# Performance work log

Measured on AMD Instinct MI355X. Metric: run time of the kernel, lower is better.

The kernel has to match this reference:

```python
import jax, jax.numpy as jnp
import numpy as np

N = 30000
F_IN = 500
HID = 16
OUT = 3
E = 960000


def setup_inputs() -> dict:
    key = jax.random.key(0)
    ks = jax.random.split(key, 10)
    x = jax.random.normal(ks[0], (N, F_IN), dtype=jnp.float32)
    edge_index = jax.random.randint(ks[1], (2, E), 0, N, dtype=jnp.int32)
    # CNN params (torch Conv1d: weight [out, in, k], bias [out])
    s1 = 1.0 / np.sqrt(1 * 3)
    s2 = 1.0 / np.sqrt(HID * 3)
    conv1_w = jax.random.uniform(ks[2], (HID, 1, 3), jnp.float32, -s1, s1)
    conv1_b = jax.random.uniform(ks[3], (HID,), jnp.float32, -s1, s1)
    conv2_w = jax.random.uniform(ks[4], (HID, HID, 3), jnp.float32, -s2, s2)
    conv2_b = jax.random.uniform(ks[5], (HID,), jnp.float32, -s2, s2)
    # GCNConv params (glorot weight [in, out], zero bias)
    g1 = np.sqrt(6.0 / (HID + HID))
    g2 = np.sqrt(6.0 / (HID + OUT))
    gcn1_w = jax.random.uniform(ks[6], (HID, HID), jnp.float32, -g1, g1)
    gcn1_b = jnp.zeros((HID,), jnp.float32)
    gcn2_w = jax.random.uniform(ks[7], (HID, OUT), jnp.float32, -g2, g2)
    gcn2_b = jnp.zeros((OUT,), jnp.float32)
    return {"x": x, "conv1_w": conv1_w, "conv1_b": conv1_b,
            "conv2_w": conv2_w, "conv2_b": conv2_b,
            "gcn1_w": gcn1_w, "gcn1_b": gcn1_b,
            "gcn2_w": gcn2_w, "gcn2_b": gcn2_b,
            "edge_index": edge_index}


def _conv1d(x, w, b):
    # x: [N, C_in, L], w: [C_out, C_in, 3], padding=1
    y = jax.lax.conv_general_dilated(
        x, w, window_strides=(1,), padding=[(1, 1)],
        dimension_numbers=("NCH", "OIH", "NCH"))
    return y + b[None, :, None]


def _gcn_conv(x, w, b, src, dst, n):
    # x: [n, d_in] -> [n, d_out]; Kipf normalization with self-loops
    h = x @ w
    loop = jnp.arange(n, dtype=src.dtype)
    s = jnp.concatenate([src, loop])
    d = jnp.concatenate([dst, loop])
    deg = jax.ops.segment_sum(jnp.ones_like(d, dtype=h.dtype), d, num_segments=n)
    dinv = jnp.where(deg > 0, jax.lax.rsqrt(deg), 0.0)
    norm = dinv[s] * dinv[d]                      # [E+n]
    msg = h[s] * norm[:, None]                    # gather + scale
    return jax.ops.segment_sum(msg, d, num_segments=n) + b


def reference(x, conv1_w, conv1_b, conv2_w, conv2_b,
              gcn1_w, gcn1_b, gcn2_w, gcn2_b, edge_index):
    # CNN feature extractor over feature axis
    h = x[:, None, :]                             # [N, 1, F_IN]
    h = jax.nn.relu(_conv1d(h, conv1_w, conv1_b))  # [N, HID, F_IN]
    h = jax.nn.relu(_conv1d(h, conv2_w, conv2_b))  # [N, HID, F_IN]
    h = jnp.max(h, axis=2)                        # global max pool -> [N, HID]
    # GCN
    src, dst = edge_index[0], edge_index[1]
    n = h.shape[0]
    h = jax.nn.relu(_gcn_conv(h, gcn1_w, gcn1_b, src, dst, n))
    h = _gcn_conv(h, gcn2_w, gcn2_b, src, dst, n)  # [N, OUT]
    return jax.nn.log_softmax(h, axis=1)
```

## Files before the change

### kernel.cpp

```cpp
#include <hip/hip_runtime.h>
#include <hip/hip_bf16.h>

#define N_NODES 30000
#define F_INLEN 500
#define HID 16
#define OUTC 3
#define NEDGE 960000
#define YPITCH 20
#define NBIN 938
#define HBLK 128
#define EPRH (NEDGE / HBLK)
#define ECAP 1536
#define NPB2 235

typedef float  f32x4 __attribute__((ext_vector_type(4)));
typedef float  f32x2 __attribute__((ext_vector_type(2)));
typedef short  s16x8 __attribute__((ext_vector_type(8)));

static __device__ __forceinline__ unsigned short f2bf(float f) {
    unsigned int u = __float_as_uint(f);
    unsigned int r = (u + 0x7fffu + ((u >> 16) & 1u)) >> 16;
    return (unsigned short)r;
}
static __device__ __forceinline__ unsigned int pack_bf16x2(float v0, float v1) {
#if __has_builtin(__builtin_amdgcn_cvt_pk_bf16_f32)
    typedef __bf16 bf16x2_t __attribute__((ext_vector_type(2)));
    union { bf16x2_t v; unsigned int u; } cv;
    cv.v = __builtin_amdgcn_cvt_pk_bf16_f32(v0, v1);
    return cv.u;
#else
    return __builtin_amdgcn_perm(__float_as_uint(v1), __float_as_uint(v0), 0x07060302);
#endif
}

__global__ void setup_kernel(const float* __restrict__ w2, short* __restrict__ bfragsG,
                             int* __restrict__ degi)
{
    const int tid = threadIdx.x;
    const int gid = blockIdx.x * 256 + tid;
    if (gid < N_NODES) degi[gid] = 0;
    if (blockIdx.x == 0 && tid < 64) {
        const int n16 = tid & 15, q = tid >> 4;
#pragma unroll
        for (int j = 0; j < 8; j++) {
            {
                const int c = q * 8 + j;
                const int t = c >> 4, i = c & 15;
                bfragsG[tid * 16 + j] = (short)f2bf(w2[n16 * 48 + i * 3 + t]);
            }
            {
                const int c = 32 + q * 8 + j;
                short v = 0;
                if (c < 48) { const int t = c >> 4, i = c & 15; v = (short)f2bf(w2[n16 * 48 + i * 3 + t]); }
                bfragsG[tid * 16 + 8 + j] = v;
            }
        }
    }
}

__global__ __launch_bounds__(256, 7) void conv_hist(
    const float* __restrict__ x,
    const float* __restrict__ w1, const float* __restrict__ b1,
    const float* __restrict__ b2, const short* __restrict__ bfragsG,
    const int* __restrict__ dst, int* __restrict__ degi,
    int* __restrict__ cntbase, float* __restrict__ h0)
{
    __shared__ __align__(16) float xp[502];
    __shared__ __align__(16) unsigned short yh[516 * YPITCH];
    __shared__ float red[64];

    const int tid = threadIdx.x;

    if (blockIdx.x < HBLK) {
        int* histH = (int*)yh;
        for (int i = tid; i < NBIN; i += 256) histH[i] = 0;
        __syncthreads();
        const int e0 = blockIdx.x * EPRH;
        for (int e = e0 + tid; e < e0 + EPRH; e += 256) {
            const int d = dst[e];
            atomicAdd(&histH[d >> 5], 1);
            atomicAdd(&degi[d], 1);
        }
        __syncthreads();
        for (int i = tid; i < NBIN; i += 256) cntbase[blockIdx.x * NBIN + i] = histH[i];
        return;
    }

    const int node = blockIdx.x - HBLK;
    const int lane = tid & 63;
    const int wave = tid >> 6;
    const int n16  = lane & 15;
    const int q    = lane >> 4;

    if (tid == 0) { xp[0] = 0.f; xp[501] = 0.f; }
    if (tid < 125) {
        const float4 v = ((const float4*)(x + (long long)node * F_INLEN))[tid];
        xp[4 * tid + 1] = v.x; xp[4 * tid + 2] = v.y;
        xp[4 * tid + 3] = v.z; xp[4 * tid + 4] = v.w;
    }
    {
        const int ri = tid >> 4;
        const int row = (ri == 0) ? 0 : (500 + ri);
        yh[row * YPITCH + (tid & 15)] = 0;
    }
    const s16x8* bfp = (const s16x8*)(bfragsG + lane * 16);
    const s16x8 bh0 = bfp[0], bh1 = bfp[1];

    f32x2 wt0[8], wt1[8], wt2[8], bb[8];
#pragma unroll
    for (int cp = 0; cp < 8; cp++) {
        const int c0 = 2 * cp, c1 = 2 * cp + 1;
        wt0[cp] = (f32x2){w1[c0 * 3 + 0], w1[c1 * 3 + 0]};
        wt1[cp] = (f32x2){w1[c0 * 3 + 1], w1[c1 * 3 + 1]};
        wt2[cp] = (f32x2){w1[c0 * 3 + 2], w1[c1 * 3 + 2]};
        bb[cp]  = (f32x2){b1[c0], b1[c1]};
    }
    __syncthreads();

    for (int p = tid; p < 500; p += 256) {
        const float x0 = xp[p], x1 = xp[p + 1], x2 = xp[p + 2];
        const f32x2 xv0 = {x0, x0}, xv1 = {x1, x1}, xv2 = {x2, x2};
        const f32x2 zero = {0.f, 0.f};
        unsigned int hp[8];
#pragma unroll
        for (int cp = 0; cp < 8; cp++) {
            f32x2 a = bb[cp];
            a = __builtin_elementwise_fma(wt0[cp], xv0, a);
            a = __builtin_elementwise_fma(wt1[cp], xv1, a);
            a = __builtin_elementwise_fma(wt2[cp], xv2, a);
            a = __builtin_elementwise_max(a, zero);
            hp[cp] = pack_bf16x2(a[0], a[1]);
        }
        uint2* d = (uint2*)&yh[(p + 1) * YPITCH];
        d[0] = make_uint2(hp[0], hp[1]);
        d[1] = make_uint2(hp[2], hp[3]);
        d[2] = make_uint2(hp[4], hp[5]);
        d[3] = make_uint2(hp[6], hp[7]);
    }
    __syncthreads();

    struct S8 { short4 lo, hi; };
    float mx0 = -3.0e38f, mx1 = -3.0e38f, mx2 = -3.0e38f, mx3 = -3.0e38f;
#pragma unroll
    for (int it = 0; it < 8; it++) {
        const int tile = wave * 8 + it;
        const int p0 = tile * 16 + n16;
        const int cA = (q & 1) * 8;
        const int rA = p0 + (q >> 1);
        const int rB = p0 + 2 + (q >> 1);
        S8 t0, t1;
        t0.lo = *(const short4*)&yh[rA * YPITCH + cA];
        t0.hi = *(const short4*)&yh[rA * YPITCH + cA + 4];
        t1.lo = *(const short4*)&yh[rB * YPITCH + cA];
        t1.hi = *(const short4*)&yh[rB * YPITCH + cA + 4];
        const s16x8 ah0 = *(const s16x8*)&t0;
        const s16x8 ah1 = *(const s16x8*)&t1;
        f32x4 acc = {0.f, 0.f, 0.f, 0.f};
        acc = __builtin_amdgcn_mfma_f32_16x16x32_bf16(ah0, bh0, acc, 0, 0, 0);
        acc = __builtin_amdgcn_mfma_f32_16x16x32_bf16(ah1, bh1, acc, 0, 0, 0);
        if (it < 7) {
            mx0 = fmaxf(mx0, acc[0]);
            mx1 = fmaxf(mx1, acc[1]);
            mx2 = fmaxf(mx2, acc[2]);
            mx3 = fmaxf(mx3, acc[3]);
        } else if (wave < 3) {
            mx0 = fmaxf(mx0, acc[0]);
            mx1 = fmaxf(mx1, acc[1]);
            mx2 = fmaxf(mx2, acc[2]);
            mx3 = fmaxf(mx3, acc[3]);
        } else if (q == 0) {
            mx0 = fmaxf(mx0, acc[0]);
            mx1 = fmaxf(mx1, acc[1]);
            mx2 = fmaxf(mx2, acc[2]);
            mx3 = fmaxf(mx3, acc[3]);
        }
    }
    float m = fmaxf(fmaxf(mx0, mx1), fmaxf(mx2, mx3));
    m = fmaxf(m, __shfl_xor(m, 16));
    m = fmaxf(m, __shfl_xor(m, 32));
    if (lane < 16) red[wave * 16 + lane] = m;
    __syncthreads();
    if (tid < 16) {
        const float mm = fmaxf(fmaxf(red[tid], red[16 + tid]), fmaxf(red[32 + tid], red[48 + tid]));
        h0[node * HID + tid] = fmaxf(mm + b2[tid], 0.f);
    }
}

__global__ __launch_bounds__(512) void reorder2(
    const int* __restrict__ src, const int* __restrict__ dst,
    const int* __restrict__ cntbase, int* __restrict__ packed,
    int* __restrict__ binstart, const int* __restrict__ degi,
    float* __restrict__ dinv, float* __restrict__ h0)
{
    __shared__ int2 sc2A[NBIN], sc2B[NBIN];
    __shared__ int gexc[NBIN];
    __shared__ int lexc[NBIN];
    __shared__ int cursor[NBIN];
    __shared__ int srt[EPRH];
    const int tid = threadIdx.x;
    const int blk = blockIdx.x;

    for (int bin = tid; bin < NBIN; bin += 512) {
        int tot = 0, psum = 0, lc = 0;
        for (int k = 0; k < HBLK; k++) {
            const int c = cntbase[k * NBIN + bin];
            tot += c;
            if (k < blk) psum += c;
            if (k == blk) lc = c;
        }
        cursor[bin] = tot;
        gexc[bin]   = psum;
        lexc[bin]   = lc;
        sc2A[bin]   = make_int2(tot, lc);
    }
    __syncthreads();
    {
        int2* pA = sc2A; int2* pB = sc2B;
        for (int off = 1; off < NBIN; off <<= 1) {
            for (int i = tid; i < NBIN; i += 512) {
                int2 v = pA[i];
                if (i >= off) { const int2 u = pA[i - off]; v.x += u.x; v.y += u.y; }
                pB[i] = v;
            }
            __syncthreads();
            int2* tp = pA; pA = pB; pB = tp;
        }
        for (int i = tid; i < NBIN; i += 512) {
            const int tot = cursor[i];
            const int lc  = lexc[i];
            const int et  = pA[i].x - tot;
            const int el  = pA[i].y - lc;
            gexc[i] += et;
            if (blk == 0) binstart[i] = et;
            lexc[i]   = el;
            cursor[i] = el;
        }
        if (blk == 0 && tid == 0) binstart[NBIN] = NEDGE;
    }
    __syncthreads();
    const int e0 = blk * EPRH;
    for (int e = e0 + tid; e < e0 + EPRH; e += 512) {
        const int d = dst[e];
        const int bin = d >> 5;
        const int pos = atomicAdd(&cursor[bin], 1);
        srt[pos] = src[e] | (d << 15);
    }
    __syncthreads();
    for (int i = tid; i < EPRH; i += 512) {
        const int bin = srt[i] >> 20;
        packed[gexc[bin] + (i - lexc[bin])] = srt[i];
    }
    const int n0 = blk * NPB2;
    for (int n = n0 + tid; n < n0 + NPB2 && n < N_NODES; n += 512) {
        const float dv = rsqrtf((float)(degi[n] + 1));
        dinv[n] = dv;
        f32x4* h4 = (f32x4*)(h0 + n * HID);
#pragma unroll
        for (int k = 0; k < 4; k++) h4[k] = h4[k] * dv;
    }
}

__global__ __launch_bounds__(256) void agg1_kernel(
    const int* __restrict__ binstart, const int* __restrict__ packed,
    const float* __restrict__ h0,
    const float* __restrict__ W1, const float* __restrict__ b1g,
    const float* __restrict__ W2, float4* __restrict__ t2p4)
{
    __shared__ float w1s[256];
    __shared__ float w2s[48];
    __shared__ float b1s[16];
    __shared__ float accS[32 * 17];
    __shared__ int eL[ECAP];
    __shared__ int srt[ECAP];
    __shared__ int h32[32], ls32[32], lofs32[32];
    const int tid = threadIdx.x;
    const int blk = blockIdx.x;
    w1s[tid] = W1[tid];
    if (tid < 48) w2s[tid] = W2[tid];
    if (tid < 16) b1s[tid] = b1g[tid];
    if (tid < 32) h32[tid] = 0;
    const int beg = binstart[blk];
    const int cnt = binstart[blk + 1] - beg;
    __syncthreads();
    for (int j = tid; j < cnt; j += 256) {
        const int p = packed[beg + j];
        eL[j] = p;
        atomicAdd(&h32[(p >> 15) & 31], 1);
    }
    __syncthreads();
    if (tid < 32) {
        const int v = h32[tid];
        int inc = v;
#pragma unroll
        for (int off = 1; off < 32; off <<= 1) {
            const int y = __shfl_up(inc, off);
            if (tid >= off) inc += y;
        }
        ls32[tid] = inc - v;
        lofs32[tid] = inc - v;
    }
    __syncthreads();
    for (int j = tid; j < cnt; j += 256) {
        const int p = eL[j];
        const int pos = atomicAdd(&lofs32[(p >> 15) & 31], 1);
        srt[pos] = p;
    }
    __syncthreads();
    const int n = tid >> 3;
    const int eslot = (tid >> 2) & 1;
    const int q = tid & 3;
    const int node = blk * 32 + n;
    const bool valid = node < N_NODES;
    f32x4 acc = {0.f, 0.f, 0.f, 0.f};
    if (valid) {
        const int s0 = ls32[n];
        const int s1 = s0 + h32[n];
        for (int i = s0 + eslot; i < s1; i += 2) {
            const int s = srt[i] & 32767;
            acc += *(const f32x4*)(h0 + s * HID + q * 4);
        }
    }
#pragma unroll
    for (int c = 0; c < 4; c++) acc[c] += __shfl_xor(acc[c], 4);
    if (valid && eslot == 0) {
        acc += *(const f32x4*)(h0 + node * HID + q * 4);
        accS[n * 17 + q * 4 + 0] = acc[0];
        accS[n * 17 + q * 4 + 1] = acc[1];
        accS[n * 17 + q * 4 + 2] = acc[2];
        accS[n * 17 + q * 4 + 3] = acc[3];
    }
    __syncthreads();
    if (tid < 128) {
        const int n2 = tid >> 2;
        const int node2 = blk * 32 + n2;
        if (node2 < N_NODES) {
            const float dv = rsqrtf((float)(h32[n2] + 1));
            const int q2 = tid & 3;
            float y0 = 0.f, y1 = 0.f, y2 = 0.f, y3 = 0.f;
#pragma unroll
            for (int i = 0; i < 16; i++) {
                const float a = accS[n2 * 17 + i];
                y0 = fmaf(a, w1s[i * 16 + q2 * 4 + 0], y0);
                y1 = fmaf(a, w1s[i * 16 + q2 * 4 + 1], y1);
                y2 = fmaf(a, w1s[i * 16 + q2 * 4 + 2], y2);
                y3 = fmaf(a, w1s[i * 16 + q2 * 4 + 3], y3);
            }
            float d0 = 0.f, d1 = 0.f, d2 = 0.f;
            const float yv[4] = {y0, y1, y2, y3};
#pragma unroll
            for (int j = 0; j < 4; j++) {
                const int o = q2 * 4 + j;
                const float h = fmaxf(b1s[o] + dv * yv[j], 0.f);
                d0 = fmaf(h, w2s[o * 3 + 0], d0);
                d1 = fmaf(h, w2s[o * 3 + 1], d1);
                d2 = fmaf(h, w2s[o * 3 + 2], d2);
            }
            d0 += __shfl_xor(d0, 1); d0 += __shfl_xor(d0, 2);
            d1 += __shfl_xor(d1, 1); d1 += __shfl_xor(d1, 2);
            d2 += __shfl_xor(d2, 1); d2 += __shfl_xor(d2, 2);
            if (q2 == 0) t2p4[node2] = make_float4(d0 * dv, d1 * dv, d2 * dv, dv);
        }
    }
}

__global__ __launch_bounds__(256) void agg2_kernel(
    const int* __restrict__ binstart, const int* __restrict__ packed,
    const float4* __restrict__ t2p4,
    const float* __restrict__ b2g, float* __restrict__ out)
{
    __shared__ float acc2[32 * 5];
    const int tid = threadIdx.x;
    const int blk = blockIdx.x;
    for (int i = tid; i < 32 * 5; i += 256) acc2[i] = 0.f;
    const int beg = binstart[blk];
    const int end = binstart[blk + 1];
    __syncthreads();
    for (int j = beg + tid; j < end; j += 256) {
        const int p = packed[j];
        const int s = p & 32767;
        const int dl = (p >> 15) & 31;
        const float4 v = t2p4[s];
        atomicAdd(&acc2[dl * 5 + 0], v.x);
        atomicAdd(&acc2[dl * 5 + 1], v.y);
        atomicAdd(&acc2[dl * 5 + 2], v.z);
    }
    __syncthreads();
    if (tid < 32) {
        const int node = blk * 32 + tid;
        if (node < N_NODES) {
            const float4 self = t2p4[node];
            const float dv = self.w;
            const float z0 = b2g[0] + dv * (acc2[tid * 5 + 0] + self.x);
            const float z1 = b2g[1] + dv * (acc2[tid * 5 + 1] + self.y);
            const float z2 = b2g[2] + dv * (acc2[tid * 5 + 2] + self.z);
            const float m = fmaxf(z0, fmaxf(z1, z2));
            const float lg = m + logf(expf(z0 - m) + expf(z1 - m) + expf(z2 - m));
            out[node * 3 + 0] = z0 - lg;
            out[node * 3 + 1] = z1 - lg;
            out[node * 3 + 2] = z2 - lg;
        }
    }
}

extern "C" void kernel_launch(void* const* d_in, const int* in_sizes, int n_in,
                              void* d_out, int out_size, void* d_ws, size_t ws_size,
                              hipStream_t stream)
{
    const float* x   = (const float*)d_in[0];
    const float* w1  = (const float*)d_in[1];
    const float* b1  = (const float*)d_in[2];
    const float* w2  = (const float*)d_in[3];
    const float* b2  = (const float*)d_in[4];
    const float* g1w = (const float*)d_in[5];
    const float* g1b = (const float*)d_in[6];
    const float* g2w = (const float*)d_in[7];
    const float* g2b = (const float*)d_in[8];
    const int*   ei  = (const int*)d_in[9];
    const int* src = ei;
    const int* dst = ei + NEDGE;

    float* ws = (float*)d_ws;
    float*  h0      = ws;
    float*  dinv    = ws + 480000;
    float4* t2p4    = (float4*)(ws + 510000);
    int*    degi    = (int*)(ws + 630000);
    int*    cntbase = (int*)(ws + 660000);
    int*    binstart= (int*)(ws + 780064);
    int*    packed  = (int*)(ws + 781024);
    short*  bfragsG = (short*)(ws + 1741024);
    float*  out     = (float*)d_out;

    setup_kernel<<<118, 256, 0, stream>>>(w2, bfragsG, degi);
    conv_hist<<<HBLK + N_NODES, 256, 0, stream>>>(x, w1, b1, b2, bfragsG,
                                                  dst, degi, cntbase, h0);
    reorder2<<<HBLK, 512, 0, stream>>>(src, dst, cntbase, packed, binstart,
                                       degi, dinv, h0);
    agg1_kernel<<<NBIN, 256, 0, stream>>>(binstart, packed, h0,
                                          g1w, g1b, g2w, t2p4);
    agg2_kernel<<<NBIN, 256, 0, stream>>>(binstart, packed, t2p4, g2b, out);
}
```

Before: 234.4 us.

## Reuse agg1's per-bin destination sort in agg2 to replace shared atomics

agg1 now writes its locally sorted edge list back to the packed buffer and stores each bin's per-node offsets and counts. agg2 then reads these and does a per-node gather with 8 lanes per node and a shuffle reduction, instead of scattering into shared memory with float atomics. The degree zeroing moves from the setup kernel to hipMemsetAsync, and the setup kernel shrinks to one 64-thread block. The cost is extra global writes in agg1 and one more memset call.

```diff
diff --git a/kernel.cpp b/kernel.cpp
--- a/kernel.cpp
+++ b/kernel.cpp
@@ -33,27 +33,22 @@
 #endif
 }
 
-__global__ void setup_kernel(const float* __restrict__ w2, short* __restrict__ bfragsG,
-                             int* __restrict__ degi)
+__global__ void setup_kernel(const float* __restrict__ w2, short* __restrict__ bfragsG)
 {
     const int tid = threadIdx.x;
-    const int gid = blockIdx.x * 256 + tid;
-    if (gid < N_NODES) degi[gid] = 0;
-    if (blockIdx.x == 0 && tid < 64) {
-        const int n16 = tid & 15, q = tid >> 4;
-#pragma unroll
-        for (int j = 0; j < 8; j++) {
-            {
-                const int c = q * 8 + j;
-                const int t = c >> 4, i = c & 15;
-                bfragsG[tid * 16 + j] = (short)f2bf(w2[n16 * 48 + i * 3 + t]);
-            }
-            {
-                const int c = 32 + q * 8 + j;
-                short v = 0;
-                if (c < 48) { const int t = c >> 4, i = c & 15; v = (short)f2bf(w2[n16 * 48 + i * 3 + t]); }
-                bfragsG[tid * 16 + 8 + j] = v;
-            }
+    const int n16 = tid & 15, q = tid >> 4;
+#pragma unroll
+    for (int j = 0; j < 8; j++) {
+        {
+            const int c = q * 8 + j;
+            const int t = c >> 4, i = c & 15;
+            bfragsG[tid * 16 + j] = (short)f2bf(w2[n16 * 48 + i * 3 + t]);
+        }
+        {
+            const int c = 32 + q * 8 + j;
+            short v = 0;
+            if (c < 48) { const int t = c >> 4, i = c & 15; v = (short)f2bf(w2[n16 * 48 + i * 3 + t]); }
+            bfragsG[tid * 16 + 8 + j] = v;
         }
     }
 }
@@ -261,10 +256,11 @@
 }
 
 __global__ __launch_bounds__(256) void agg1_kernel(
-    const int* __restrict__ binstart, const int* __restrict__ packed,
+    const int* __restrict__ binstart, int* __restrict__ packed,
     const float* __restrict__ h0,
     const float* __restrict__ W1, const float* __restrict__ b1g,
-    const float* __restrict__ W2, float4* __restrict__ t2p4)
+    const float* __restrict__ W2, float4* __restrict__ t2p4,
+    int* __restrict__ binofs)
 {
     __shared__ float w1s[256];
     __shared__ float w2s[48];
@@ -306,6 +302,11 @@
         srt[pos] = p;
     }
     __syncthreads();
+    for (int j = tid; j < cnt; j += 256) packed[beg + j] = srt[j];
+    if (tid < 32) {
+        binofs[blk * 64 + tid]      = ls32[tid];
+        binofs[blk * 64 + 32 + tid] = h32[tid];
+    }
     const int n = tid >> 3;
     const int eslot = (tid >> 2) & 1;
     const int q = tid & 3;
@@ -365,40 +366,48 @@
 
 __global__ __launch_bounds__(256) void agg2_kernel(
     const int* __restrict__ binstart, const int* __restrict__ packed,
-    const float4* __restrict__ t2p4,
+    const float4* __restrict__ t2p4, const int* __restrict__ binofs,
     const float* __restrict__ b2g, float* __restrict__ out)
 {
-    __shared__ float acc2[32 * 5];
+    __shared__ int eL[ECAP];
+    __shared__ int ofs[64];
     const int tid = threadIdx.x;
     const int blk = blockIdx.x;
-    for (int i = tid; i < 32 * 5; i += 256) acc2[i] = 0.f;
     const int beg = binstart[blk];
-    const int end = binstart[blk + 1];
-    __syncthreads();
-    for (int j = beg + tid; j < end; j += 256) {
-        const int p = packed[j];
-        const int s = p & 32767;
-        const int dl = (p >> 15) & 31;
-        const float4 v = t2p4[s];
-        atomicAdd(&acc2[dl * 5 + 0], v.x);
-        atomicAdd(&acc2[dl * 5 + 1], v.y);
-        atomicAdd(&acc2[dl * 5 + 2], v.z);
-    }
-    __syncthreads();
-    if (tid < 32) {
-        const int node = blk * 32 + tid;
-        if (node < N_NODES) {
-            const float4 self = t2p4[node];
-            const float dv = self.w;
-            const float z0 = b2g[0] + dv * (acc2[tid * 5 + 0] + self.x);
-            const float z1 = b2g[1] + dv * (acc2[tid * 5 + 1] + self.y);
-            const float z2 = b2g[2] + dv * (acc2[tid * 5 + 2] + self.z);
-            const float m = fmaxf(z0, fmaxf(z1, z2));
-            const float lg = m + logf(expf(z0 - m) + expf(z1 - m) + expf(z2 - m));
-            out[node * 3 + 0] = z0 - lg;
-            out[node * 3 + 1] = z1 - lg;
-            out[node * 3 + 2] = z2 - lg;
-        }
+    const int cnt = binstart[blk + 1] - beg;
+    if (tid < 64) ofs[tid] = binofs[blk * 64 + tid];
+    for (int j = tid; j < cnt; j += 256) eL[j] = packed[beg + j];
+    __syncthreads();
+    const int n = tid >> 3;
+    const int ln8 = tid & 7;
+    const int node = blk * 32 + n;
+    float a0 = 0.f, a1 = 0.f, a2 = 0.f;
+    if (node < N_NODES) {
+        const int s0 = ofs[n];
+        const int s1 = s0 + ofs[32 + n];
+        for (int i = s0 + ln8; i < s1; i += 8) {
+            const int s = eL[i] & 32767;
+            const float4 v = t2p4[s];
+            a0 += v.x; a1 += v.y; a2 += v.z;
+        }
+    }
+#pragma unroll
+    for (int msk = 1; msk < 8; msk <<= 1) {
+        a0 += __shfl_xor(a0, msk);
+        a1 += __shfl_xor(a1, msk);
+        a2 += __shfl_xor(a2, msk);
+    }
+    if (ln8 == 0 && node < N_NODES) {
+        const float4 self = t2p4[node];
+        const float dv = self.w;
+        const float z0 = b2g[0] + dv * (a0 + self.x);
+        const float z1 = b2g[1] + dv * (a1 + self.y);
+        const float z2 = b2g[2] + dv * (a2 + self.z);
+        const float m = fmaxf(z0, fmaxf(z1, z2));
+        const float lg = m + logf(expf(z0 - m) + expf(z1 - m) + expf(z2 - m));
+        out[node * 3 + 0] = z0 - lg;
+        out[node * 3 + 1] = z1 - lg;
+        out[node * 3 + 2] = z2 - lg;
     }
 }
 
@@ -427,15 +436,17 @@
     int*    cntbase = (int*)(ws + 660000);
     int*    binstart= (int*)(ws + 780064);
     int*    packed  = (int*)(ws + 781024);
-    short*  bfragsG = (short*)(ws + 1741024);
+    int*    binofs  = (int*)(ws + 1741024);
+    short*  bfragsG = (short*)(ws + 1801056);
     float*  out     = (float*)d_out;
 
-    setup_kernel<<<118, 256, 0, stream>>>(w2, bfragsG, degi);
+    hipMemsetAsync(degi, 0, N_NODES * sizeof(int), stream);
+    setup_kernel<<<1, 64, 0, stream>>>(w2, bfragsG);
     conv_hist<<<HBLK + N_NODES, 256, 0, stream>>>(x, w1, b1, b2, bfragsG,
                                                   dst, degi, cntbase, h0);
     reorder2<<<HBLK, 512, 0, stream>>>(src, dst, cntbase, packed, binstart,
                                        degi, dinv, h0);
     agg1_kernel<<<NBIN, 256, 0, stream>>>(binstart, packed, h0,
-                                          g1w, g1b, g2w, t2p4);
-    agg2_kernel<<<NBIN, 256, 0, stream>>>(binstart, packed, t2p4, g2b, out);
-}
+                                          g1w, g1b, g2w, t2p4, binofs);
+    agg2_kernel<<<NBIN, 256, 0, stream>>>(binstart, packed, t2p4, binofs, g2b, out);
+}
```

Result: faster. 229.5 us (-2.1%).
